# Performance work log

Hardware: AMD Instinct MI355X
Metric: run time of the kernel (lower is better)

Reference implementation:

```python
import jax, jax.numpy as jnp
import numpy as np
import math

EMBED_DIM = 1024
NUM_HEADS = 16
PROJ_DIM = 1024
HEAD_DIM = PROJ_DIM // NUM_HEADS  # 64
ALPHA = 0.3  # warmup_steps=0, step_count irrelevant -> alpha_eff = alpha
DIFFUSION_STEPS = 2


def setup_inputs() -> dict:
    key = jax.random.key(0)
    ks = jax.random.split(key, 9)
    B, N, D = 1, 2048, EMBED_DIM
    s_in = 1.0 / math.sqrt(D)
    s_p = 1.0 / math.sqrt(PROJ_DIM)
    return {
        "hidden_states": jax.random.normal(ks[0], (B, N, D), dtype=jnp.float32),
        # Linear weights stored as [in, out] (apply as x @ W + b)
        "Wq": jax.random.normal(ks[1], (D, PROJ_DIM), dtype=jnp.float32) * s_in,
        "bq": jax.random.normal(ks[2], (PROJ_DIM,), dtype=jnp.float32) * s_in,
        "Wk": jax.random.normal(ks[3], (D, PROJ_DIM), dtype=jnp.float32) * s_in,
        "bk": jax.random.normal(ks[4], (PROJ_DIM,), dtype=jnp.float32) * s_in,
        "Wv": jax.random.normal(ks[5], (D, PROJ_DIM), dtype=jnp.float32) * s_in,
        "bv": jax.random.normal(ks[6], (PROJ_DIM,), dtype=jnp.float32) * s_in,
        "Wo": jax.random.normal(ks[7], (PROJ_DIM, D), dtype=jnp.float32) * s_p,
        "bo": jax.random.normal(ks[8], (D,), dtype=jnp.float32) * s_p,
    }


def reference(hidden_states, Wq, bq, Wk, bk, Wv, bv, Wo, bo):
    B, N, D = hidden_states.shape
    H, hd = NUM_HEADS, HEAD_DIM

    def split_heads(x):  # [B, N, P] -> [B, H, N, hd]
        return x.reshape(B, -1, H, hd).transpose(0, 2, 1, 3)

    Q = split_heads(hidden_states @ Wq + bq)
    K = split_heads(hidden_states @ Wk + bk)
    V = split_heads(hidden_states @ Wv + bv)

    # scores: note original uses (sqrt(hd) + 1e-8) denominator here
    scores = jnp.einsum("bhqd,bhkd->bhqk", Q, K) / (math.sqrt(hd) + 1e-8)
    p0 = jax.nn.softmax(scores, axis=-1)

    # key-transition matrix P: exact sqrt(hd) denominator
    sim = jnp.einsum("bhid,bhjd->bhij", K, K) / math.sqrt(hd)
    P = jax.nn.softmax(sim, axis=-1)

    # iterative diffusion, unrolled (early-stop can only fire after the
    # final update when diffusion_steps=2, so output is identical)
    a = ALPHA
    p = p0
    for _ in range(DIFFUSION_STEPS):
        p = (1.0 - a) * p0 + a * jnp.einsum("bhqn,bhnm->bhqm", p, P)

    attn = jnp.einsum("bhqk,bhkd->bhqd", p, V)
    attn = attn.transpose(0, 2, 1, 3).reshape(B, N, PROJ_DIM)
    out = attn @ Wo + bo
    return out, p
```

## Files before the change

### kernel.cpp

```cpp
#include <hip/hip_runtime.h>


typedef __attribute__((ext_vector_type(8))) short bf16x8;
typedef __attribute__((ext_vector_type(4))) short s16x4;
typedef __attribute__((ext_vector_type(4))) float f32x4;

constexpr int N_TOK   = 2048;
constexpr int N_HEADS = 16;
constexpr int HD      = 64;
constexpr int EMB     = 1024;

#define DEVINL __device__ __forceinline__

DEVINL unsigned short f2bf_u(float f) {
  unsigned x = __float_as_uint(f);
  return (unsigned short)((x + 0x7fffu + ((x >> 16) & 1u)) >> 16);
}
DEVINL float bf2f_u(unsigned short h) { return __uint_as_float(((unsigned)h) << 16); }

DEVINL void async16(const void* src, void* dst) {
  __builtin_amdgcn_global_load_lds(
      (const __attribute__((address_space(1))) void*)src,
      (__attribute__((address_space(3))) void*)dst, 16, 0, 0);
}

enum : int { EPI_F32SCALE = 0, EPI_F32BIAS, EPI_BF16, EPI_QKSPLIT, EPI_VSPLIT,
             EPI_DIFF_BF16, EPI_DIFF_F32, EPI_SM_ROW, EPI_SM_COL };

__global__ __launch_bounds__(256)
void gemm_stats(const unsigned short* __restrict__ Am, long long sAz,
                const unsigned short* __restrict__ Bm, long long sBz,
                float alpha, float* __restrict__ mxo, float* __restrict__ iso)
{
  __shared__ __align__(16) char smem[3 * 16384];
  __shared__ float lred[2][2][128];
  const int tid = threadIdx.x, lane = tid & 63, wv = tid >> 6;
  const int wr = wv >> 1, wc = wv & 1, l15 = lane & 15, g = lane >> 4;
  const size_t z = blockIdx.y;
  const unsigned short* Az = Am + z * (size_t)sAz + (size_t)blockIdx.x * 128 * HD;
  const unsigned short* Bz = Bm + z * (size_t)sBz;
  const int cbs = (tid & 7) * 16;
  const int rr = tid >> 3;

  #pragma unroll
  for (int i = 0; i < 4; ++i) {
    const int r = i * 32 + rr;
    async16((const char*)Az + (size_t)r * 128 + (cbs ^ ((r & 7) << 4)),
            smem + i * 4096 + wv * 1024);
  }
  #pragma unroll
  for (int i = 0; i < 4; ++i) {
    const int r = i * 32 + rr;
    async16((const char*)Bz + (size_t)r * 128 + (cbs ^ ((r & 7) << 4)),
            smem + 16384 + i * 4096 + wv * 1024);
  }
  __syncthreads();

  float rm[4][4], rs[4][4];
  #pragma unroll
  for (int m = 0; m < 4; ++m)
    #pragma unroll
    for (int j = 0; j < 4; ++j) { rm[m][j] = -3.0e38f; rs[m][j] = 0.f; }

  for (int ct = 0; ct < 16; ++ct) {
    const int cur = ct & 1;
    if (ct + 1 < 16) {
      const int nb = cur ^ 1;
      #pragma unroll
      for (int i = 0; i < 4; ++i) {
        const int r = i * 32 + rr;
        const size_t br = (size_t)(ct + 1) * 128 + r;
        async16((const char*)Bz + br * 128 + (cbs ^ ((r & 7) << 4)),
                smem + 16384 + nb * 16384 + i * 4096 + wv * 1024);
      }
    }
    f32x4 acc[4][4];
    #pragma unroll
    for (int m = 0; m < 4; ++m)
      #pragma unroll
      for (int n = 0; n < 4; ++n) acc[m][n] = f32x4{0.f, 0.f, 0.f, 0.f};
    #pragma unroll
    for (int kk = 0; kk < 2; ++kk) {
      bf16x8 a[4], b[4];
      #pragma unroll
      for (int m = 0; m < 4; ++m) {
        const int row = wr * 64 + m * 16 + l15;
        const int c = (kk * 64 + g * 16) ^ ((row & 7) << 4);
        a[m] = *(const bf16x8*)(smem + row * 128 + c);
      }
      #pragma unroll
      for (int n = 0; n < 4; ++n) {
        const int row = wc * 64 + n * 16 + l15;
        const int c = (kk * 64 + g * 16) ^ ((row & 7) << 4);
        b[n] = *(const bf16x8*)(smem + 16384 + cur * 16384 + row * 128 + c);
      }
      #pragma unroll
      for (int m = 0; m < 4; ++m)
        #pragma unroll
        for (int n = 0; n < 4; ++n)
          acc[m][n] = __builtin_amdgcn_mfma_f32_16x16x32_bf16(a[m], b[n], acc[m][n], 0, 0, 0);
    }
    #pragma unroll
    for (int m = 0; m < 4; ++m)
    #pragma unroll
    for (int j = 0; j < 4; ++j) {
      const float v0 = acc[m][0][j] * alpha, v1 = acc[m][1][j] * alpha;
      const float v2 = acc[m][2][j] * alpha, v3 = acc[m][3][j] * alpha;
      const float pm = fmaxf(fmaxf(v0, v1), fmaxf(v2, v3));
      const float nm = fmaxf(rm[m][j], pm);
      rs[m][j] = rs[m][j] * expf(rm[m][j] - nm)
               + expf(v0 - nm) + expf(v1 - nm) + expf(v2 - nm) + expf(v3 - nm);
      rm[m][j] = nm;
    }
    __syncthreads();
  }

  #pragma unroll
  for (int off = 1; off < 16; off <<= 1) {
    #pragma unroll
    for (int m = 0; m < 4; ++m)
    #pragma unroll
    for (int j = 0; j < 4; ++j) {
      const float om = __shfl_xor(rm[m][j], off);
      const float os = __shfl_xor(rs[m][j], off);
      const float nm = fmaxf(rm[m][j], om);
      rs[m][j] = rs[m][j] * expf(rm[m][j] - nm) + os * expf(om - nm);
      rm[m][j] = nm;
    }
  }
  if (l15 == 0) {
    #pragma unroll
    for (int m = 0; m < 4; ++m)
    #pragma unroll
    for (int j = 0; j < 4; ++j) {
      const int r = wr * 64 + m * 16 + g * 4 + j;
      lred[0][wc][r] = rm[m][j];
      lred[1][wc][r] = rs[m][j];
    }
  }
  __syncthreads();
  if (tid < 128) {
    const float m0 = lred[0][0][tid], m1 = lred[0][1][tid];
    const float M = fmaxf(m0, m1);
    const float S = lred[1][0][tid] * expf(m0 - M) + lred[1][1][tid] * expf(m1 - M);
    mxo[z * N_TOK + (size_t)blockIdx.x * 128 + tid] = M;
    iso[z * N_TOK + (size_t)blockIdx.x * 128 + tid] = 1.0f / S;
  }
}

template<int EPI>
__global__ __launch_bounds__(512, 2)
void gemm256_diff(const unsigned short* __restrict__ Am, int lda, long long sAz,
                  const unsigned short* __restrict__ Bm, int ldb, long long sBz,
                  int K,
                  const unsigned short* __restrict__ P0, int ldp0, long long sPz,
                  void* __restrict__ Cv, int ldc, long long sCz)
{
  __shared__ __align__(16) char smem[2 * 65536];
  const int tid  = threadIdx.x;
  const int lane = tid & 63, wv = tid >> 6;
  const int wr = wv >> 2, wc = wv & 3;
  const int l15 = lane & 15, g = lane >> 4;
  const int z = blockIdx.z;
  const size_t brow = (size_t)blockIdx.y * 256;
  const size_t bcol = (size_t)blockIdx.x * 256;

  const unsigned short* Ab = Am + (size_t)z * (size_t)sAz;
  const unsigned short* Bb = Bm + (size_t)z * (size_t)sBz;
  const int NT = K >> 6;

  const int cbs = (tid & 7) * 16;
  const int r00 = (tid >> 3),       r01 = 64  + (tid >> 3);
  const int r10 = 128 + (tid >> 3), r11 = 192 + (tid >> 3);
  const char* gA00 = (const char*)Ab + ((brow + r00) * (size_t)lda) * 2 + (cbs ^ ((r00 & 7) << 4));
  const char* gA01 = (const char*)Ab + ((brow + r01) * (size_t)lda) * 2 + (cbs ^ ((r01 & 7) << 4));
  const char* gA10 = (const char*)Ab + ((brow + r10) * (size_t)lda) * 2 + (cbs ^ ((r10 & 7) << 4));
  const char* gA11 = (const char*)Ab + ((brow + r11) * (size_t)lda) * 2 + (cbs ^ ((r11 & 7) << 4));
  const char* gB00 = (const char*)Bb + ((bcol + r00) * (size_t)ldb) * 2 + (cbs ^ ((r00 & 7) << 4));
  const char* gB01 = (const char*)Bb + ((bcol + r01) * (size_t)ldb) * 2 + (cbs ^ ((r01 & 7) << 4));
  const char* gB10 = (const char*)Bb + ((bcol + r10) * (size_t)ldb) * 2 + (cbs ^ ((r10 & 7) << 4));
  const char* gB11 = (const char*)Bb + ((bcol + r11) * (size_t)ldb) * 2 + (cbs ^ ((r11 & 7) << 4));

  f32x4 acc[8][4];
  #pragma unroll
  for (int m = 0; m < 8; ++m)
    #pragma unroll
    for (int n = 0; n < 4; ++n) acc[m][n] = f32x4{0.f, 0.f, 0.f, 0.f};

  auto ldA = [&](int cur, int mf, int kk) -> bf16x8 {
    const int row = wr * 128 + mf * 16 + l15;
    const int c = (kk * 64 + g * 16) ^ ((row & 7) << 4);
    return *(const bf16x8*)(smem + cur * 65536 + row * 128 + c);
  };
  auto ldB = [&](int cur, int nf, int kk) -> bf16x8 {
    const int row = wc * 64 + nf * 16 + l15;
    const int c = (kk * 64 + g * 16) ^ ((row & 7) << 4);
    return *(const bf16x8*)(smem + cur * 65536 + 32768 + row * 128 + c);
  };

  {
    char* d0 = smem;
    async16(gA00, d0 +             wv * 1024);
    async16(gA01, d0 +  8192 +     wv * 1024);
    async16(gA10, d0 + 16384 +     wv * 1024);
    async16(gA11, d0 + 24576 +     wv * 1024);
    async16(gB00, d0 + 32768 +     wv * 1024);
    async16(gB01, d0 + 40960 +     wv * 1024);
    async16(gB10, d0 + 49152 +     wv * 1024);
    async16(gB11, d0 + 57344 +     wv * 1024);
    if (NT > 1) {
      char* d1 = smem + 65536 + 32768;
      async16(gB00 + 128, d1 +             wv * 1024);
      async16(gB01 + 128, d1 +  8192 +     wv * 1024);
      async16(gB10 + 128, d1 + 16384 +     wv * 1024);
      async16(gB11 + 128, d1 + 24576 +     wv * 1024);
      asm volatile("s_waitcnt vmcnt(4)" ::: "memory");
    } else {
      asm volatile("s_waitcnt vmcnt(0)" ::: "memory");
    }
    __builtin_amdgcn_sched_barrier(0);
    __builtin_amdgcn_s_barrier();
  }

#define READA(P, Q)                                                       \
    bf16x8 P##00 = ldA(cur, 2*(Q),   0), P##01 = ldA(cur, 2*(Q),   1),    \
           P##10 = ldA(cur, 2*(Q)+1, 0), P##11 = ldA(cur, 2*(Q)+1, 1);

#define MFMA16(P, Q)                                                                        \
    __builtin_amdgcn_s_setprio(1);                                                          \
    acc[2*(Q)+0][0] = __builtin_amdgcn_mfma_f32_16x16x32_bf16(P##00, b00, acc[2*(Q)+0][0], 0, 0, 0); \
    acc[2*(Q)+0][1] = __builtin_amdgcn_mfma_f32_16x16x32_bf16(P##00, b10, acc[2*(Q)+0][1], 0, 0, 0); \
    acc[2*(Q)+0][2] = __builtin_amdgcn_mfma_f32_16x16x32_bf16(P##00, b20, acc[2*(Q)+0][2], 0, 0, 0); \
    acc[2*(Q)+0][3] = __builtin_amdgcn_mfma_f32_16x16x32_bf16(P##00, b30, acc[2*(Q)+0][3], 0, 0, 0); \
    acc[2*(Q)+1][0] = __builtin_amdgcn_mfma_f32_16x16x32_bf16(P##10, b00, acc[2*(Q)+1][0], 0, 0, 0); \
    acc[2*(Q)+1][1] = __builtin_amdgcn_mfma_f32_16x16x32_bf16(P##10, b10, acc[2*(Q)+1][1], 0, 0, 0); \
    acc[2*(Q)+1][2] = __builtin_amdgcn_mfma_f32_16x16x32_bf16(P##10, b20, acc[2*(Q)+1][2], 0, 0, 0); \
    acc[2*(Q)+1][3] = __builtin_amdgcn_mfma_f32_16x16x32_bf16(P##10, b30, acc[2*(Q)+1][3], 0, 0, 0); \
    acc[2*(Q)+0][0] = __builtin_amdgcn_mfma_f32_16x16x32_bf16(P##01, b01, acc[2*(Q)+0][0], 0, 0, 0); \
    acc[2*(Q)+0][1] = __builtin_amdgcn_mfma_f32_16x16x32_bf16(P##01, b11, acc[2*(Q)+0][1], 0, 0, 0); \
    acc[2*(Q)+0][2] = __builtin_amdgcn_mfma_f32_16x16x32_bf16(P##01, b21, acc[2*(Q)+0][2], 0, 0, 0); \
    acc[2*(Q)+0][3] = __builtin_amdgcn_mfma_f32_16x16x32_bf16(P##01, b31, acc[2*(Q)+0][3], 0, 0, 0); \
    acc[2*(Q)+1][0] = __builtin_amdgcn_mfma_f32_16x16x32_bf16(P##11, b01, acc[2*(Q)+1][0], 0, 0, 0); \
    acc[2*(Q)+1][1] = __builtin_amdgcn_mfma_f32_16x16x32_bf16(P##11, b11, acc[2*(Q)+1][1], 0, 0, 0); \
    acc[2*(Q)+1][2] = __builtin_amdgcn_mfma_f32_16x16x32_bf16(P##11, b21, acc[2*(Q)+1][2], 0, 0, 0); \
    acc[2*(Q)+1][3] = __builtin_amdgcn_mfma_f32_16x16x32_bf16(P##11, b31, acc[2*(Q)+1][3], 0, 0, 0); \
    __builtin_amdgcn_s_setprio(0);

#define SB __builtin_amdgcn_sched_barrier(0)

  int cur = 0;
  for (int t = 0; t < NT; ++t, cur ^= 1) {
    const int o = cur ^ 1;
    const size_t ko1 = (size_t)(t + 1) * 128;
    const size_t ko2 = (size_t)(t + 2) * 128;
    bf16x8 b00 = ldB(cur, 0, 0), b01 = ldB(cur, 0, 1);
    bf16x8 b10 = ldB(cur, 1, 0), b11 = ldB(cur, 1, 1);
    bf16x8 b20 = ldB(cur, 2, 0), b21 = ldB(cur, 2, 1);
    bf16x8 b30 = ldB(cur, 3, 0), b31 = ldB(cur, 3, 1);
    READA(f0_, 0)
    READA(f1_, 1)
    if (t + 1 < NT) {
      char* d = smem + o * 65536;
      async16(gA00 + ko1, d +        wv * 1024);
      async16(gA01 + ko1, d + 8192 + wv * 1024);
    }
    asm volatile("s_waitcnt lgkmcnt(4)" ::: "memory");
    SB;
    MFMA16(f0_, 0)
    READA(f2_, 2)
    if (t + 1 < NT) {
      char* d = smem + o * 65536;
      async16(gA10 + ko1, d + 16384 + wv * 1024);
      async16(gA11 + ko1, d + 24576 + wv * 1024);
    }
    asm volatile("s_waitcnt lgkmcnt(4)" ::: "memory");
    SB;
    MFMA16(f1_, 1)
    SB;
    __builtin_amdgcn_s_barrier();
    READA(f3_, 3)
    if (t + 2 < NT) {
      char* d = smem + cur * 65536 + 32768;
      async16(gB00 + ko2, d +        wv * 1024);
      async16(gB01 + ko2, d + 8192 + wv * 1024);
    }
    asm volatile("s_waitcnt lgkmcnt(4)" ::: "memory");
    SB;
    MFMA16(f2_, 2)
    if (t + 2 < NT) {
      char* d = smem + cur * 65536 + 32768 + 16384;
      async16(gB10 + ko2, d +        wv * 1024);
      async16(gB11 + ko2, d + 8192 + wv * 1024);
    }
    asm volatile("s_waitcnt lgkmcnt(0)" ::: "memory");
    SB;
    MFMA16(f3_, 3)
    if (t + 1 < NT) {
      if (t + 2 < NT) asm volatile("s_waitcnt vmcnt(4)" ::: "memory");
      else            asm volatile("s_waitcnt vmcnt(0)" ::: "memory");
      SB;
      __builtin_amdgcn_s_barrier();
    }
  }
#undef MFMA16
#undef READA
#undef SB

  float* Cf = (float*)Cv + (size_t)z * (size_t)sCz;
  unsigned short* Cu = (unsigned short*)Cv + (size_t)z * (size_t)sCz;
  const unsigned short* P0z = P0 + (size_t)z * (size_t)sPz;
  #pragma unroll
  for (int m = 0; m < 8; ++m)
  #pragma unroll
  for (int n = 0; n < 4; ++n)
  #pragma unroll
  for (int j = 0; j < 4; ++j) {
    const size_t R = brow + (size_t)(wr * 128 + m * 16 + g * 4 + j);
    const size_t C = bcol + (size_t)(wc * 64 + n * 16 + l15);
    const float v = acc[m][n][j];
    const float p0v = bf2f_u(P0z[R * (size_t)ldp0 + C]);
    const float r = 0.7f * p0v + 0.3f * v;
    if constexpr (EPI == EPI_DIFF_BF16) Cu[R * ldc + C] = f2bf_u(r);
    else                                Cf[R * ldc + C] = r;
  }
}

template<int BM, int BN, bool AF32, int EPI>
__global__ __launch_bounds__(256)
void gemm_tn(const void* __restrict__ Av, int lda, long long sAz,
             const unsigned short* __restrict__ Bm, int ldb, long long sBz,
             int K, float alpha, const float* __restrict__ bias,
             const float* __restrict__ mxp, const float* __restrict__ isp,
             const unsigned short* __restrict__ P0, int ldp0, long long sPz,
             void* __restrict__ Cv, int ldc, long long sCz)
{
  constexpr int BKk = 64;
  constexpr int WM = BM / 2, WN = BN / 2, MF = WM / 16, NF = WN / 16;
  constexpr int AES = AF32 ? 4 : 2;
  constexpr int ABYTES = BM * BKk * AES, BBYTES = BN * BKk * 2;
  __shared__ __align__(16) char smem[ABYTES + BBYTES];

  const int tid  = threadIdx.x;
  const int lane = tid & 63, wv = tid >> 6;
  const int wr = wv >> 1, wc = wv & 1;
  const int l15 = lane & 15, g = lane >> 4;
  const int z = blockIdx.z;
  const size_t brow = (size_t)blockIdx.y * BM;
  const size_t bcol = (size_t)blockIdx.x * BN;

  const char* Ab = (const char*)Av + (size_t)z * (size_t)sAz * AES;
  const unsigned short* Bb = Bm + (size_t)z * (size_t)sBz;

  f32x4 acc[MF][NF];
  #pragma unroll
  for (int m = 0; m < MF; ++m)
    #pragma unroll
    for (int n = 0; n < NF; ++n)
      acc[m][n] = f32x4{0.f, 0.f, 0.f, 0.f};

  constexpr int EPC_A = AF32 ? 4 : 8;
  constexpr int CPR_A = BKk / EPC_A;
  constexpr int IT_A  = (BM * CPR_A) / 256;
  constexpr int CPR_B = 8;
  constexpr int IT_B  = (BN * CPR_B) / 256;

  for (int k0 = 0; k0 < K; k0 += BKk) {
    #pragma unroll
    for (int i = 0; i < IT_A; ++i) {
      const int c   = i * 256 + wv * 64 + lane;
      const int row = c / CPR_A;
      const int eo  = (c % CPR_A) * EPC_A;
      const char* src = Ab + ((brow + row) * (size_t)lda + (size_t)(k0 + eo)) * AES;
      async16(src, smem + (size_t)(i * 256 + wv * 64) * 16);
    }
    #pragma unroll
    for (int i = 0; i < IT_B; ++i) {
      const int c   = i * 256 + wv * 64 + lane;
      const int row = c / CPR_B;
      const int eo  = (c % CPR_B) * 8;
      const unsigned short* src = Bb + (bcol + row) * (size_t)ldb + (size_t)(k0 + eo);
      async16(src, smem + ABYTES + (size_t)(i * 256 + wv * 64) * 16);
    }
    __syncthreads();
    #pragma unroll
    for (int kk = 0; kk < 2; ++kk) {
      bf16x8 a[MF], b[NF];
      #pragma unroll
      for (int m = 0; m < MF; ++m) {
        const int r = wr * WM + m * 16 + l15;
        if constexpr (!AF32) {
          a[m] = *(const bf16x8*)(smem + ((size_t)r * BKk + kk * 32 + g * 8) * 2);
        } else {
          const float* pa = (const float*)smem + (size_t)r * BKk + kk * 32 + g * 8;
          const f32x4 lo = *(const f32x4*)pa;
          const f32x4 hi = *(const f32x4*)(pa + 4);
          bf16x8 t;
          t[0] = (short)f2bf_u(lo[0]); t[1] = (short)f2bf_u(lo[1]);
          t[2] = (short)f2bf_u(lo[2]); t[3] = (short)f2bf_u(lo[3]);
          t[4] = (short)f2bf_u(hi[0]); t[5] = (short)f2bf_u(hi[1]);
          t[6] = (short)f2bf_u(hi[2]); t[7] = (short)f2bf_u(hi[3]);
          a[m] = t;
        }
      }
      #pragma unroll
      for (int n = 0; n < NF; ++n) {
        const int cc = wc * WN + n * 16 + l15;
        b[n] = *(const bf16x8*)(smem + ABYTES + ((size_t)cc * BKk + kk * 32 + g * 8) * 2);
      }
      #pragma unroll
      for (int m = 0; m < MF; ++m)
        #pragma unroll
        for (int n = 0; n < NF; ++n)
          acc[m][n] = __builtin_amdgcn_mfma_f32_16x16x32_bf16(a[m], b[n], acc[m][n], 0, 0, 0);
    }
    __syncthreads();
  }

  float* Cf = (float*)Cv + (size_t)z * (size_t)sCz;
  unsigned short* Cu = (unsigned short*)Cv + (size_t)z * (size_t)sCz;

  #pragma unroll
  for (int m = 0; m < MF; ++m)
  #pragma unroll
  for (int n = 0; n < NF; ++n)
  #pragma unroll
  for (int j = 0; j < 4; ++j) {
    const size_t R  = brow + (size_t)(wr * WM + m * 16 + g * 4 + j);
    const size_t Cc = bcol + (size_t)(wc * WN + n * 16 + l15);
    const float v = acc[m][n][j];
    if constexpr (EPI == EPI_F32SCALE) {
      Cf[R * ldc + Cc] = v * alpha;
    } else if constexpr (EPI == EPI_F32BIAS) {
      Cf[R * ldc + Cc] = v + bias[Cc];
    } else if constexpr (EPI == EPI_BF16) {
      Cu[R * ldc + Cc] = f2bf_u(v);
    } else if constexpr (EPI == EPI_QKSPLIT) {
      const float t = v + bias[Cc];
      Cu[(Cc >> 6) * ((size_t)N_TOK * HD) + R * HD + (Cc & 63)] = f2bf_u(t);
    } else if constexpr (EPI == EPI_VSPLIT) {
      const float t = v + bias[Cc];
      Cu[(Cc >> 6) * ((size_t)HD * N_TOK) + (Cc & 63) * (size_t)N_TOK + R] = f2bf_u(t);
    } else if constexpr (EPI == EPI_DIFF_BF16) {
      const unsigned short* P0z = P0 + (size_t)z * (size_t)sPz;
      const float p0v = bf2f_u(P0z[R * (size_t)ldp0 + Cc]);
      Cu[R * ldc + Cc] = f2bf_u(0.7f * p0v + 0.3f * v);
    } else if constexpr (EPI == EPI_DIFF_F32) {
      const unsigned short* P0z = P0 + (size_t)z * (size_t)sPz;
      const float p0v = bf2f_u(P0z[R * (size_t)ldp0 + Cc]);
      Cf[R * ldc + Cc] = 0.7f * p0v + 0.3f * v;
    } else if constexpr (EPI == EPI_SM_ROW) {
      const float M = mxp[(size_t)z * N_TOK + R];
      const float S = isp[(size_t)z * N_TOK + R];
      Cu[R * ldc + Cc] = f2bf_u(expf(v * alpha - M) * S);
    } else if constexpr (EPI == EPI_SM_COL) {
      const float M = mxp[(size_t)z * N_TOK + Cc];
      const float S = isp[(size_t)z * N_TOK + Cc];
      Cu[R * ldc + Cc] = f2bf_u(expf(v * alpha - M) * S);
    }
  }
  (void)alpha; (void)bias; (void)mxp; (void)isp; (void)P0; (void)ldp0;
}

__global__ __launch_bounds__(256)
void row_softmax(const float* __restrict__ S, long long sS,
                 unsigned short* __restrict__ O, long long sO)
{
  __shared__ float red[8];
  const int tid = threadIdx.x;
  const size_t row = blockIdx.x;
  const size_t h = blockIdx.y;
  const f32x4* Sr = (const f32x4*)(S + (size_t)h * sS + row * N_TOK);
  f32x4 v0 = Sr[tid], v1 = Sr[tid + 256];
  float m = fmaxf(fmaxf(fmaxf(v0[0], v0[1]), fmaxf(v0[2], v0[3])),
                  fmaxf(fmaxf(v1[0], v1[1]), fmaxf(v1[2], v1[3])));
  #pragma unroll
  for (int o = 32; o; o >>= 1) m = fmaxf(m, __shfl_xor(m, o));
  if ((tid & 63) == 0) red[tid >> 6] = m;
  __syncthreads();
  m = fmaxf(fmaxf(red[0], red[1]), fmaxf(red[2], red[3]));
  f32x4 e0, e1;
  #pragma unroll
  for (int k = 0; k < 4; ++k) { e0[k] = expf(v0[k] - m); e1[k] = expf(v1[k] - m); }
  float s = e0[0]+e0[1]+e0[2]+e0[3]+e1[0]+e1[1]+e1[2]+e1[3];
  #pragma unroll
  for (int o = 32; o; o >>= 1) s += __shfl_xor(s, o);
  if ((tid & 63) == 0) red[4 + (tid >> 6)] = s;
  __syncthreads();
  s = red[4] + red[5] + red[6] + red[7];
  const float inv = 1.0f / s;
  s16x4 o0, o1;
  #pragma unroll
  for (int k = 0; k < 4; ++k) {
    o0[k] = (short)f2bf_u(e0[k] * inv);
    o1[k] = (short)f2bf_u(e1[k] * inv);
  }
  s16x4* Or = (s16x4*)(O + (size_t)h * sO + row * N_TOK);
  Or[tid] = o0; Or[tid + 256] = o1;
}

__global__ __launch_bounds__(256)
void row_reduce(const float* __restrict__ S, long long sS,
                float* __restrict__ mx, float* __restrict__ is_)
{
  __shared__ float red[8];
  const int tid = threadIdx.x;
  const size_t row = blockIdx.x;
  const size_t h = blockIdx.y;
  const f32x4* Sr = (const f32x4*)(S + (size_t)h * sS + row * N_TOK);
  f32x4 v0 = Sr[tid], v1 = Sr[tid + 256];
  float m = fmaxf(fmaxf(fmaxf(v0[0], v0[1]), fmaxf(v0[2], v0[3])),
                  fmaxf(fmaxf(v1[0], v1[1]), fmaxf(v1[2], v1[3])));
  #pragma unroll
  for (int o = 32; o; o >>= 1) m = fmaxf(m, __shfl_xor(m, o));
  if ((tid & 63) == 0) red[tid >> 6] = m;
  __syncthreads();
  m = fmaxf(fmaxf(red[0], red[1]), fmaxf(red[2], red[3]));
  float s = 0.f;
  #pragma unroll
  for (int k = 0; k < 4; ++k) { s += expf(v0[k] - m); s += expf(v1[k] - m); }
  #pragma unroll
  for (int o = 32; o; o >>= 1) s += __shfl_xor(s, o);
  if ((tid & 63) == 0) red[4 + (tid >> 6)] = s;
  __syncthreads();
  s = red[4] + red[5] + red[6] + red[7];
  if (tid == 0) { mx[h * N_TOK + row] = m; is_[h * N_TOK + row] = 1.0f / s; }
}

__global__ __launch_bounds__(256)
void pt_write(const float* __restrict__ S, long long sS,
              const float* __restrict__ mx, const float* __restrict__ is_,
              unsigned short* __restrict__ PT, long long sP)
{
  const int tid = threadIdx.x;
  const size_t row = blockIdx.x;
  const size_t h = blockIdx.y;
  const f32x4* Sr = (const f32x4*)(S + (size_t)h * sS + row * N_TOK);
  const f32x4* M4 = (const f32x4*)(mx + h * N_TOK);
  const f32x4* I4 = (const f32x4*)(is_ + h * N_TOK);
  s16x4* Pr = (s16x4*)(PT + (size_t)h * sP + row * N_TOK);
  #pragma unroll
  for (int i = 0; i < 2; ++i) {
    const int idx = tid + i * 256;
    f32x4 sv = Sr[idx], mv = M4[idx], iv = I4[idx];
    s16x4 o;
    #pragma unroll
    for (int k = 0; k < 4; ++k) o[k] = (short)f2bf_u(expf(sv[k] - mv[k]) * iv[k]);
    Pr[idx] = o;
  }
}

__global__ __launch_bounds__(256)
void transpose_cast4(const float* __restrict__ w0, const float* __restrict__ w1,
                     const float* __restrict__ w2, const float* __restrict__ w3,
                     unsigned short* __restrict__ o0, unsigned short* __restrict__ o1,
                     unsigned short* __restrict__ o2, unsigned short* __restrict__ o3)
{
  __shared__ float tile[64][65];
  const float* in; unsigned short* out;
  if      (blockIdx.z == 0) { in = w0; out = o0; }
  else if (blockIdx.z == 1) { in = w1; out = o1; }
  else if (blockIdx.z == 2) { in = w2; out = o2; }
  else                      { in = w3; out = o3; }
  const int n = EMB;
  const int bx = blockIdx.x * 64, by = blockIdx.y * 64;
  const int tid = threadIdx.x;
  const int r = tid >> 2;
  const int q = tid & 3;
  #pragma unroll
  for (int i = 0; i < 4; ++i) {
    const int c = q * 16 + i * 4;
    f32x4 v = *(const f32x4*)(in + (size_t)(by + r) * n + bx + c);
    tile[r][c + 0] = v[0]; tile[r][c + 1] = v[1];
    tile[r][c + 2] = v[2]; tile[r][c + 3] = v[3];
  }
  __syncthreads();
  #pragma unroll
  for (int i = 0; i < 4; ++i) {
    const int c0 = q * 16 + i * 4;
    s16x4 o;
    o[0] = (short)f2bf_u(tile[c0 + 0][r]); o[1] = (short)f2bf_u(tile[c0 + 1][r]);
    o[2] = (short)f2bf_u(tile[c0 + 2][r]); o[3] = (short)f2bf_u(tile[c0 + 3][r]);
    *(s16x4*)(out + (size_t)(bx + r) * n + by + c0) = o;
  }
}

__global__ __launch_bounds__(256)
void cast_f32_bf16(const float* __restrict__ in, unsigned short* __restrict__ out)
{
  const size_t i = (size_t)blockIdx.x * 256 + threadIdx.x;
  f32x4 v = ((const f32x4*)in)[i];
  s16x4 o;
  o[0] = (short)f2bf_u(v[0]); o[1] = (short)f2bf_u(v[1]);
  o[2] = (short)f2bf_u(v[2]); o[3] = (short)f2bf_u(v[3]);
  ((s16x4*)out)[i] = o;
}

extern "C" void kernel_launch(void* const* d_in, const int* in_sizes, int n_in,
                              void* d_out, int out_size, void* d_ws, size_t ws_size,
                              hipStream_t stream)
{
  (void)in_sizes; (void)n_in; (void)out_size;
  const float* hs = (const float*)d_in[0];
  const float* Wq = (const float*)d_in[1];
  const float* bq = (const float*)d_in[2];
  const float* Wk = (const float*)d_in[3];
  const float* bk = (const float*)d_in[4];
  const float* Wv = (const float*)d_in[5];
  const float* bv = (const float*)d_in[6];
  const float* Wo = (const float*)d_in[7];
  const float* bo = (const float*)d_in[8];

  float* outO = (float*)d_out;
  float* outP = outO + (size_t)N_TOK * EMB;

  const long long NN = (long long)N_TOK * N_TOK;
  const long long sH = (long long)N_TOK * HD;

  const bool batched = ws_size >= ((size_t)440 << 20);
  const int PH = batched ? N_HEADS : 1;

  char* ws = (char*)d_ws;
  auto alloc = [&](size_t b) { char* p = ws; ws += (b + 255) & ~(size_t)255; return p; };
  unsigned short* Xbf = (unsigned short*)alloc((size_t)N_TOK * EMB * 2);
  unsigned short* WqT = (unsigned short*)alloc((size_t)EMB * EMB * 2);
  unsigned short* WkT = (unsigned short*)alloc((size_t)EMB * EMB * 2);
  unsigned short* WvT = (unsigned short*)alloc((size_t)EMB * EMB * 2);
  unsigned short* WoT = (unsigned short*)alloc((size_t)EMB * EMB * 2);
  unsigned short* Qb  = (unsigned short*)alloc((size_t)N_HEADS * N_TOK * HD * 2);
  unsigned short* Kb  = (unsigned short*)alloc((size_t)N_HEADS * N_TOK * HD * 2);
  unsigned short* Vt  = (unsigned short*)alloc((size_t)N_HEADS * N_TOK * HD * 2);
  unsigned short* attn= (unsigned short*)alloc((size_t)N_TOK * EMB * 2);
  float* mxq = (float*)alloc((size_t)N_HEADS * N_TOK * 4);
  float* isq = (float*)alloc((size_t)N_HEADS * N_TOK * 4);
  float* mxk = (float*)alloc((size_t)N_HEADS * N_TOK * 4);
  float* isk = (float*)alloc((size_t)N_HEADS * N_TOK * 4);
  unsigned short* p0b = (unsigned short*)alloc((size_t)PH * NN * 2);
  unsigned short* PT  = (unsigned short*)alloc((size_t)PH * NN * 2);
  unsigned short* p1b = (unsigned short*)alloc((size_t)PH * NN * 2);

  cast_f32_bf16<<<dim3(N_TOK * EMB / 1024), 256, 0, stream>>>(hs, Xbf);
  transpose_cast4<<<dim3(16, 16, 4), 256, 0, stream>>>(Wq, Wk, Wv, Wo, WqT, WkT, WvT, WoT);

  gemm_tn<128, 128, false, EPI_QKSPLIT><<<dim3(EMB / 128, N_TOK / 128, 1), 256, 0, stream>>>(
      Xbf, EMB, 0, WqT, EMB, 0, EMB, 0.f, bq, nullptr, nullptr, nullptr, 0, 0, Qb, 0, 0);
  gemm_tn<128, 128, false, EPI_QKSPLIT><<<dim3(EMB / 128, N_TOK / 128, 1), 256, 0, stream>>>(
      Xbf, EMB, 0, WkT, EMB, 0, EMB, 0.f, bk, nullptr, nullptr, nullptr, 0, 0, Kb, 0, 0);
  gemm_tn<128, 128, false, EPI_VSPLIT><<<dim3(EMB / 128, N_TOK / 128, 1), 256, 0, stream>>>(
      Xbf, EMB, 0, WvT, EMB, 0, EMB, 0.f, bv, nullptr, nullptr, nullptr, 0, 0, Vt, 0, 0);

  if (batched) {
    gemm_stats<<<dim3(16, N_HEADS), 256, 0, stream>>>(Qb, sH, Kb, sH, 0.125f, mxq, isq);
    gemm_tn<128, 128, false, EPI_SM_ROW><<<dim3(16, 16, N_HEADS), 256, 0, stream>>>(
        Qb, HD, sH, Kb, HD, sH, HD, 0.125f, nullptr, mxq, isq, nullptr, 0, 0, p0b, N_TOK, NN);
    gemm_stats<<<dim3(16, N_HEADS), 256, 0, stream>>>(Kb, sH, Kb, sH, 0.125f, mxk, isk);
    gemm_tn<128, 128, false, EPI_SM_COL><<<dim3(16, 16, N_HEADS), 256, 0, stream>>>(
        Kb, HD, sH, Kb, HD, sH, HD, 0.125f, nullptr, mxk, isk, nullptr, 0, 0, PT, N_TOK, NN);
    gemm256_diff<EPI_DIFF_BF16><<<dim3(8, 8, N_HEADS), 512, 0, stream>>>(
        p0b, N_TOK, NN, PT, N_TOK, NN, N_TOK, p0b, N_TOK, NN, p1b, N_TOK, NN);
    gemm256_diff<EPI_DIFF_F32><<<dim3(8, 8, N_HEADS), 512, 0, stream>>>(
        p1b, N_TOK, NN, PT, N_TOK, NN, N_TOK, p0b, N_TOK, NN, outP, N_TOK, NN);
    gemm_tn<128, 64, true, EPI_BF16><<<dim3(1, N_TOK / 128, N_HEADS), 256, 0, stream>>>(
        outP, N_TOK, NN, Vt, N_TOK, (long long)HD * N_TOK,
        N_TOK, 0.f, nullptr, nullptr, nullptr, nullptr, 0, 0, attn, EMB, HD);
  } else {
    for (int h = 0; h < N_HEADS; ++h) {
      float* slot = outP + (size_t)h * NN;
      const unsigned short* Qh = Qb + (size_t)h * N_TOK * HD;
      const unsigned short* Kh = Kb + (size_t)h * N_TOK * HD;
      gemm_tn<128, 128, false, EPI_F32SCALE><<<dim3(16, 16, 1), 256, 0, stream>>>(
          Qh, HD, 0, Kh, HD, 0, HD, 0.125f, nullptr, nullptr, nullptr, nullptr, 0, 0, slot, N_TOK, 0);
      row_softmax<<<dim3(N_TOK, 1), 256, 0, stream>>>(slot, 0, p0b, 0);
      gemm_tn<128, 128, false, EPI_F32SCALE><<<dim3(16, 16, 1), 256, 0, stream>>>(
          Kh, HD, 0, Kh, HD, 0, HD, 0.125f, nullptr, nullptr, nullptr, nullptr, 0, 0, slot, N_TOK, 0);
      row_reduce<<<dim3(N_TOK, 1), 256, 0, stream>>>(slot, 0, mxq, isq);
      pt_write<<<dim3(N_TOK, 1), 256, 0, stream>>>(slot, 0, mxq, isq, PT, 0);
      gemm_tn<128, 128, false, EPI_DIFF_BF16><<<dim3(16, 16, 1), 256, 0, stream>>>(
          p0b, N_TOK, 0, PT, N_TOK, 0, N_TOK, 0.f, nullptr, nullptr, nullptr, p0b, N_TOK, 0, p1b, N_TOK, 0);
      gemm_tn<128, 128, false, EPI_DIFF_F32><<<dim3(16, 16, 1), 256, 0, stream>>>(
          p1b, N_TOK, 0, PT, N_TOK, 0, N_TOK, 0.f, nullptr, nullptr, nullptr, p0b, N_TOK, 0, slot, N_TOK, 0);
    }
    gemm_tn<128, 64, true, EPI_BF16><<<dim3(1, N_TOK / 128, N_HEADS), 256, 0, stream>>>(
        outP, N_TOK, NN, Vt, N_TOK, (long long)HD * N_TOK,
        N_TOK, 0.f, nullptr, nullptr, nullptr, nullptr, 0, 0, attn, EMB, HD);
  }

  gemm_tn<128, 128, false, EPI_F32BIAS><<<dim3(EMB / 128, N_TOK / 128, 1), 256, 0, stream>>>(
      attn, EMB, 0, WoT, EMB, 0, EMB, 0.f, bo, nullptr, nullptr, nullptr, 0, 0, outO, EMB, 0);
}
```

Measured before the change: 975.2 us.

## Restructure diffusion GEMM mainloop into 8-phase barrier-synchronized pipeline

Rewrites the 256x256 diffusion GEMM main loop as an unrolled pair of K-tiles, each split into four phases. Each phase issues LDS reads for one A sub-fragment, stages part of the next tile with async global-to-LDS loads, then syncs with a barrier before its MFMA block. Shared memory is reorganized into eight 16KB slots indexed by parity and wave-row/col. The goal is finer interleaving of global loads, LDS reads and MFMAs across waves, at the cost of more barriers per tile. The loop assumes NT is even.

```diff
diff --git a/kernel.cpp b/kernel.cpp
--- a/kernel.cpp
+++ b/kernel.cpp
@@ -156,7 +156,7 @@
                   const unsigned short* __restrict__ P0, int ldp0, long long sPz,
                   void* __restrict__ Cv, int ldc, long long sCz)
 {
-  __shared__ __align__(16) char smem[2 * 65536];
+  __shared__ __align__(16) char smem[8 * 16384];
   const int tid  = threadIdx.x;
   const int lane = tid & 63, wv = tid >> 6;
   const int wr = wv >> 2, wc = wv & 3;
@@ -168,18 +168,17 @@
   const unsigned short* Ab = Am + (size_t)z * (size_t)sAz;
   const unsigned short* Bb = Bm + (size_t)z * (size_t)sBz;
   const int NT = K >> 6;
+  const int NI = NT >> 1;
 
   const int cbs = (tid & 7) * 16;
-  const int r00 = (tid >> 3),       r01 = 64  + (tid >> 3);
-  const int r10 = 128 + (tid >> 3), r11 = 192 + (tid >> 3);
-  const char* gA00 = (const char*)Ab + ((brow + r00) * (size_t)lda) * 2 + (cbs ^ ((r00 & 7) << 4));
-  const char* gA01 = (const char*)Ab + ((brow + r01) * (size_t)lda) * 2 + (cbs ^ ((r01 & 7) << 4));
-  const char* gA10 = (const char*)Ab + ((brow + r10) * (size_t)lda) * 2 + (cbs ^ ((r10 & 7) << 4));
-  const char* gA11 = (const char*)Ab + ((brow + r11) * (size_t)lda) * 2 + (cbs ^ ((r11 & 7) << 4));
-  const char* gB00 = (const char*)Bb + ((bcol + r00) * (size_t)ldb) * 2 + (cbs ^ ((r00 & 7) << 4));
-  const char* gB01 = (const char*)Bb + ((bcol + r01) * (size_t)ldb) * 2 + (cbs ^ ((r01 & 7) << 4));
-  const char* gB10 = (const char*)Bb + ((bcol + r10) * (size_t)ldb) * 2 + (cbs ^ ((r10 & 7) << 4));
-  const char* gB11 = (const char*)Bb + ((bcol + r11) * (size_t)ldb) * 2 + (cbs ^ ((r11 & 7) << 4));
+  const char* gA[4];
+  const char* gB[4];
+  #pragma unroll
+  for (int i = 0; i < 4; ++i) {
+    const int r = i * 64 + (tid >> 3);
+    gA[i] = (const char*)Ab + ((brow + r) * (size_t)lda) * 2 + (cbs ^ ((r & 7) << 4));
+    gB[i] = (const char*)Bb + ((bcol + r) * (size_t)ldb) * 2 + (cbs ^ ((r & 7) << 4));
+  }
 
   f32x4 acc[8][4];
   #pragma unroll
@@ -187,44 +186,47 @@
     #pragma unroll
     for (int n = 0; n < 4; ++n) acc[m][n] = f32x4{0.f, 0.f, 0.f, 0.f};
 
-  auto ldA = [&](int cur, int mf, int kk) -> bf16x8 {
-    const int row = wr * 128 + mf * 16 + l15;
+  auto ldA = [&](int par, int mf, int kk) -> bf16x8 {
+    const int slot = par * 4 + wr;
+    const int row = mf * 16 + l15;
     const int c = (kk * 64 + g * 16) ^ ((row & 7) << 4);
-    return *(const bf16x8*)(smem + cur * 65536 + row * 128 + c);
+    return *(const bf16x8*)(smem + slot * 16384 + row * 128 + c);
   };
-  auto ldB = [&](int cur, int nf, int kk) -> bf16x8 {
-    const int row = wc * 64 + nf * 16 + l15;
+  auto ldB = [&](int par, int nf, int kk) -> bf16x8 {
+    const int slot = par * 4 + 2 + (wc >> 1);
+    const int row = (wc & 1) * 64 + nf * 16 + l15;
     const int c = (kk * 64 + g * 16) ^ ((row & 7) << 4);
-    return *(const bf16x8*)(smem + cur * 65536 + 32768 + row * 128 + c);
+    return *(const bf16x8*)(smem + slot * 16384 + row * 128 + c);
   };
 
-  {
-    char* d0 = smem;
-    async16(gA00, d0 +             wv * 1024);
-    async16(gA01, d0 +  8192 +     wv * 1024);
-    async16(gA10, d0 + 16384 +     wv * 1024);
-    async16(gA11, d0 + 24576 +     wv * 1024);
-    async16(gB00, d0 + 32768 +     wv * 1024);
-    async16(gB01, d0 + 40960 +     wv * 1024);
-    async16(gB10, d0 + 49152 +     wv * 1024);
-    async16(gB11, d0 + 57344 +     wv * 1024);
-    if (NT > 1) {
-      char* d1 = smem + 65536 + 32768;
-      async16(gB00 + 128, d1 +             wv * 1024);
-      async16(gB01 + 128, d1 +  8192 +     wv * 1024);
-      async16(gB10 + 128, d1 + 16384 +     wv * 1024);
-      async16(gB11 + 128, d1 + 24576 +     wv * 1024);
-      asm volatile("s_waitcnt vmcnt(4)" ::: "memory");
-    } else {
-      asm volatile("s_waitcnt vmcnt(0)" ::: "memory");
-    }
-    __builtin_amdgcn_sched_barrier(0);
-    __builtin_amdgcn_s_barrier();
-  }
-
-#define READA(P, Q)                                                       \
-    bf16x8 P##00 = ldA(cur, 2*(Q),   0), P##01 = ldA(cur, 2*(Q),   1),    \
-           P##10 = ldA(cur, 2*(Q)+1, 0), P##11 = ldA(cur, 2*(Q)+1, 1);
+  auto stageA = [&](int T, int h) {
+    if (T < NT) {
+      char* d = smem + ((T & 1) * 4 + h) * 16384 + wv * 1024;
+      const size_t ko = (size_t)T * 128;
+      async16(gA[2 * h] + ko,     d);
+      async16(gA[2 * h + 1] + ko, d + 8192);
+    }
+  };
+  auto stageB = [&](int T, int h) {
+    if (T < NT) {
+      char* d = smem + ((T & 1) * 4 + 2 + h) * 16384 + wv * 1024;
+      const size_t ko = (size_t)T * 128;
+      async16(gB[2 * h] + ko,     d);
+      async16(gB[2 * h + 1] + ko, d + 8192);
+    }
+  };
+
+#define SB __builtin_amdgcn_sched_barrier(0)
+
+  stageA(0, 0); stageA(0, 1); stageB(0, 0); stageB(0, 1);
+  stageB(1, 0); stageB(1, 1);
+  asm volatile("s_waitcnt vmcnt(4)" ::: "memory");
+  SB;
+  __builtin_amdgcn_s_barrier();
+
+#define READA(P, PAR, Q)                                                   \
+    bf16x8 P##00 = ldA(PAR, 2*(Q),   0), P##01 = ldA(PAR, 2*(Q),   1),     \
+           P##10 = ldA(PAR, 2*(Q)+1, 0), P##11 = ldA(PAR, 2*(Q)+1, 1);
 
 #define MFMA16(P, Q)                                                                        \
     __builtin_amdgcn_s_setprio(1);                                                          \
@@ -246,64 +248,87 @@
     acc[2*(Q)+1][3] = __builtin_amdgcn_mfma_f32_16x16x32_bf16(P##11, b31, acc[2*(Q)+1][3], 0, 0, 0); \
     __builtin_amdgcn_s_setprio(0);
 
-#define SB __builtin_amdgcn_sched_barrier(0)
-
-  int cur = 0;
-  for (int t = 0; t < NT; ++t, cur ^= 1) {
-    const int o = cur ^ 1;
-    const size_t ko1 = (size_t)(t + 1) * 128;
-    const size_t ko2 = (size_t)(t + 2) * 128;
-    bf16x8 b00 = ldB(cur, 0, 0), b01 = ldB(cur, 0, 1);
-    bf16x8 b10 = ldB(cur, 1, 0), b11 = ldB(cur, 1, 1);
-    bf16x8 b20 = ldB(cur, 2, 0), b21 = ldB(cur, 2, 1);
-    bf16x8 b30 = ldB(cur, 3, 0), b31 = ldB(cur, 3, 1);
-    READA(f0_, 0)
-    READA(f1_, 1)
-    if (t + 1 < NT) {
-      char* d = smem + o * 65536;
-      async16(gA00 + ko1, d +        wv * 1024);
-      async16(gA01 + ko1, d + 8192 + wv * 1024);
-    }
-    asm volatile("s_waitcnt lgkmcnt(4)" ::: "memory");
+#define BARRIER_LGKM0                                   \
+    SB; __builtin_amdgcn_s_barrier();                   \
+    asm volatile("s_waitcnt lgkmcnt(0)" ::: "memory");  \
     SB;
-    MFMA16(f0_, 0)
-    READA(f2_, 2)
-    if (t + 1 < NT) {
-      char* d = smem + o * 65536;
-      async16(gA10 + ko1, d + 16384 + wv * 1024);
-      async16(gA11 + ko1, d + 24576 + wv * 1024);
-    }
-    asm volatile("s_waitcnt lgkmcnt(4)" ::: "memory");
-    SB;
-    MFMA16(f1_, 1)
-    SB;
-    __builtin_amdgcn_s_barrier();
-    READA(f3_, 3)
-    if (t + 2 < NT) {
-      char* d = smem + cur * 65536 + 32768;
-      async16(gB00 + ko2, d +        wv * 1024);
-      async16(gB01 + ko2, d + 8192 + wv * 1024);
-    }
-    asm volatile("s_waitcnt lgkmcnt(4)" ::: "memory");
-    SB;
-    MFMA16(f2_, 2)
-    if (t + 2 < NT) {
-      char* d = smem + cur * 65536 + 32768 + 16384;
-      async16(gB10 + ko2, d +        wv * 1024);
-      async16(gB11 + ko2, d + 8192 + wv * 1024);
-    }
-    asm volatile("s_waitcnt lgkmcnt(0)" ::: "memory");
-    SB;
-    MFMA16(f3_, 3)
-    if (t + 1 < NT) {
-      if (t + 2 < NT) asm volatile("s_waitcnt vmcnt(4)" ::: "memory");
-      else            asm volatile("s_waitcnt vmcnt(0)" ::: "memory");
-      SB;
-      __builtin_amdgcn_s_barrier();
+
+#define ENDPHASE SB; __builtin_amdgcn_s_barrier();
+
+  for (int J = 0; J < NI; ++J) {
+    const int tE = 2 * J, tO = 2 * J + 1;
+    {
+      bf16x8 b00 = ldB(0,0,0), b01 = ldB(0,0,1), b10 = ldB(0,1,0), b11 = ldB(0,1,1);
+      bf16x8 b20 = ldB(0,2,0), b21 = ldB(0,2,1), b30 = ldB(0,3,0), b31 = ldB(0,3,1);
+      READA(p0_, 0, 0)
+      stageA(tO, 0);
+      asm volatile("s_waitcnt lgkmcnt(8)" ::: "memory");
+      BARRIER_LGKM0
+      MFMA16(p0_, 0)
+      ENDPHASE
+      {
+        READA(p1_, 0, 1)
+        stageA(tO, 1);
+        BARRIER_LGKM0
+        MFMA16(p1_, 1)
+        ENDPHASE
+      }
+      {
+        READA(p2_, 0, 2)
+        stageB(tE + 2, 0);
+        BARRIER_LGKM0
+        MFMA16(p2_, 2)
+        ENDPHASE
+      }
+      {
+        READA(p3_, 0, 3)
+        stageB(tE + 2, 1);
+        BARRIER_LGKM0
+        MFMA16(p3_, 3)
+        if (J + 1 < NI) asm volatile("s_waitcnt vmcnt(4)" ::: "memory");
+        else            asm volatile("s_waitcnt vmcnt(0)" ::: "memory");
+        ENDPHASE
+      }
+    }
+    {
+      bf16x8 b00 = ldB(1,0,0), b01 = ldB(1,0,1), b10 = ldB(1,1,0), b11 = ldB(1,1,1);
+      bf16x8 b20 = ldB(1,2,0), b21 = ldB(1,2,1), b30 = ldB(1,3,0), b31 = ldB(1,3,1);
+      READA(p4_, 1, 0)
+      stageA(tE + 2, 0);
+      asm volatile("s_waitcnt lgkmcnt(8)" ::: "memory");
+      BARRIER_LGKM0
+      MFMA16(p4_, 0)
+      ENDPHASE
+      {
+        READA(p5_, 1, 1)
+        stageA(tE + 2, 1);
+        BARRIER_LGKM0
+        MFMA16(p5_, 1)
+        ENDPHASE
+      }
+      {
+        READA(p6_, 1, 2)
+        stageB(tO + 2, 0);
+        BARRIER_LGKM0
+        MFMA16(p6_, 2)
+        ENDPHASE
+      }
+      {
+        READA(p7_, 1, 3)
+        stageB(tO + 2, 1);
+        BARRIER_LGKM0
+        MFMA16(p7_, 3)
+        if (J + 1 < NI) {
+          asm volatile("s_waitcnt vmcnt(4)" ::: "memory");
+          ENDPHASE
+        }
+      }
     }
   }
 #undef MFMA16
 #undef READA
+#undef BARRIER_LGKM0
+#undef ENDPHASE
 #undef SB
 
   float* Cf = (float*)Cv + (size_t)z * (size_t)sCz;
```

Result: no change. 993.3 us (+1.9%).
